# Kernel optimization log

Hardware: AMD Instinct MI355X
Metric: run time of the kernel (lower is better)

## Reference

```python
import jax, jax.numpy as jnp
import numpy as np

K = 512
H = 8
B = 8
T = 1024
EPS = 1e-5


def _layernorm(x, g, b):
    mu = jnp.mean(x, axis=-1, keepdims=True)
    var = jnp.var(x, axis=-1, keepdims=True)
    return (x - mu) * jax.lax.rsqrt(var + EPS) * g + b


def _attention(x, enc, wq, wk, wv, wo):
    b, t, k = x.shape
    h = H
    scale = k ** (-0.25)
    q = (x @ wq).reshape(b, t, h, k) * scale        # [b,t,h,k]
    kk = (enc @ wk).reshape(b, t, h, k) * scale
    v = (enc @ wv).reshape(b, t, h, k)
    dot = jnp.einsum('bqhd,bkhd->bhqk', q, kk)      # [b,h,t,t]
    att = jax.nn.softmax(dot, axis=-1)
    out = jnp.einsum('bhqk,bkhd->bqhd', att, v).reshape(b, t, h * k)
    return out @ wo                                  # [b,t,k]


def setup_inputs() -> dict:
    key = jax.random.key(0)
    ks = jax.random.split(key, 12)
    s = 0.02
    return {
        'x': jax.random.normal(ks[0], (B, T, K), jnp.float32),
        'enc': jax.random.normal(ks[1], (B, T, K), jnp.float32),
        'sa_wq': jax.random.normal(ks[2], (K, K * H), jnp.float32) * s,
        'sa_wk': jax.random.normal(ks[3], (K, K * H), jnp.float32) * s,
        'sa_wv': jax.random.normal(ks[4], (K, K * H), jnp.float32) * s,
        'sa_wo': jax.random.normal(ks[5], (K * H, K), jnp.float32) * s,
        'ca_wq': jax.random.normal(ks[6], (K, K * H), jnp.float32) * s,
        'ca_wk': jax.random.normal(ks[7], (K, K * H), jnp.float32) * s,
        'ca_wv': jax.random.normal(ks[8], (K, K * H), jnp.float32) * s,
        'ca_wo': jax.random.normal(ks[9], (K * H, K), jnp.float32) * s,
        'ln1_g': jnp.ones((K,), jnp.float32), 'ln1_b': jnp.zeros((K,), jnp.float32),
        'ln2_g': jnp.ones((K,), jnp.float32), 'ln2_b': jnp.zeros((K,), jnp.float32),
        'ln3_g': jnp.ones((K,), jnp.float32), 'ln3_b': jnp.zeros((K,), jnp.float32),
        'ff_w1': jax.random.normal(ks[10], (K, 4 * K), jnp.float32) * s,
        'ff_b1': jnp.zeros((4 * K,), jnp.float32),
        'ff_w2': jax.random.normal(ks[11], (4 * K, K), jnp.float32) * s,
        'ff_b2': jnp.zeros((K,), jnp.float32),
    }


def reference(x, enc, sa_wq, sa_wk, sa_wv, sa_wo, ca_wq, ca_wk, ca_wv, ca_wo,
              ln1_g, ln1_b, ln2_g, ln2_b, ln3_g, ln3_b,
              ff_w1, ff_b1, ff_w2, ff_b2):
    # masked self-attention (mask_future_steps=False -> plain self-attn)
    sa = _attention(x, x, sa_wq, sa_wk, sa_wv, sa_wo)
    x = _layernorm(sa + x, ln1_g, ln1_b)
    # encoder-decoder attention
    ca = _attention(x, enc, ca_wq, ca_wk, ca_wv, ca_wo)
    x = _layernorm(ca + x, ln2_g, ln2_b)
    # dropout p=0.0 -> identity
    ff = jax.nn.relu(x @ ff_w1 + ff_b1) @ ff_w2 + ff_b2
    x = _layernorm(ff + x, ln3_g, ln3_b)
    return x
```

## Files before the change

kernel.cpp:

```cpp
#include <hip/hip_runtime.h>
#include <stdint.h>

typedef short short8 __attribute__((ext_vector_type(8)));
typedef float f32x4 __attribute__((ext_vector_type(4)));

#define DEVI static __device__ __forceinline__

DEVI float b2f(unsigned short u) {
  union { float f; uint32_t i; } v; v.i = ((uint32_t)u) << 16; return v.f;
}
DEVI unsigned short f2b(float f) {
  union { float f; uint32_t i; } v; v.f = f;
  uint32_t r = v.i + 0x7FFFu + ((v.i >> 16) & 1u);
  return (unsigned short)(r >> 16);
}

DEVI void async_cp16(const unsigned short* g, unsigned short* l) {
  __builtin_amdgcn_global_load_lds(
      (const __attribute__((address_space(1))) void*)g,
      (__attribute__((address_space(3))) void*)l, 16, 0, 0);
}

DEVI void swz(int& bx, int& by, int& bz) {
  const int gx = gridDim.x, gy = gridDim.y, gz = gridDim.z;
  int l = blockIdx.x + gx * (blockIdx.y + gy * blockIdx.z);
  bz = l % gz; l /= gz;
  by = l % gy;
  bx = l / gy;
}


__global__ __launch_bounds__(256) void cvt_f32_bf16(
    const float4* __restrict__ src, unsigned short* __restrict__ dst) {
  const int i = blockIdx.x * 256 + threadIdx.x;
  float4 f = src[i];
  uint2 o;
  o.x = (uint32_t)f2b(f.x) | ((uint32_t)f2b(f.y) << 16);
  o.y = (uint32_t)f2b(f.z) | ((uint32_t)f2b(f.w) << 16);
  ((uint2*)dst)[i] = o;
}

__global__ __launch_bounds__(256) void wtrans(
    const float* __restrict__ src, unsigned short* __restrict__ dst, int R, int C) {
  __shared__ float tile[32][33];
  const int tx = threadIdx.x & 31, ty = threadIdx.x >> 5;
  const int c0 = blockIdx.x * 32, r0 = blockIdx.y * 32;
#pragma unroll
  for (int i = 0; i < 32; i += 8)
    tile[ty + i][tx] = src[(long)(r0 + ty + i) * C + c0 + tx];
  __syncthreads();
#pragma unroll
  for (int i = 0; i < 32; i += 8)
    dst[(long)(c0 + ty + i) * R + r0 + tx] = f2b(tile[tx][ty + i]);
}

__global__ __launch_bounds__(256) void softmax_rows(
    unsigned short* __restrict__ S, int NZ) {
  const int tid = threadIdx.x;
  const int bx = blockIdx.x;
  const long z = bx % NZ, r = bx / NZ;
  unsigned short* p = S + (z * 1024 + r) * 1024;
  float v[4];
  float m = -3.0e38f;
#pragma unroll
  for (int i = 0; i < 4; i++) { v[i] = b2f(p[tid + 256 * i]); m = fmaxf(m, v[i]); }
#pragma unroll
  for (int o = 1; o < 64; o <<= 1) m = fmaxf(m, __shfl_xor(m, o));
  __shared__ float rm[4], rsum[4];
  const int lane = tid & 63, wave = tid >> 6;
  if (lane == 0) rm[wave] = m;
  __syncthreads();
  m = fmaxf(fmaxf(rm[0], rm[1]), fmaxf(rm[2], rm[3]));
  float s = 0.f;
#pragma unroll
  for (int i = 0; i < 4; i++) { v[i] = __expf(v[i] - m); s += v[i]; }
#pragma unroll
  for (int o = 1; o < 64; o <<= 1) s += __shfl_xor(s, o);
  if (lane == 0) rsum[wave] = s;
  __syncthreads();
  s = rsum[0] + rsum[1] + rsum[2] + rsum[3];
  const float inv = 1.f / s;
#pragma unroll
  for (int i = 0; i < 4; i++) p[tid + 256 * i] = f2b(v[i] * inv);
}

__global__ __launch_bounds__(256) void layernorm_rows(
    const float* X, const float* __restrict__ g,
    const float* __restrict__ b, float* Y,
    unsigned short* __restrict__ Yb) {
  const int tid = threadIdx.x;
  const long row = blockIdx.x;
  const float* x = X + row * 512;
  float v0 = x[tid], v1 = x[tid + 256];
  float s1 = v0 + v1;
  float s2 = v0 * v0 + v1 * v1;
#pragma unroll
  for (int o = 1; o < 64; o <<= 1) {
    s1 += __shfl_xor(s1, o);
    s2 += __shfl_xor(s2, o);
  }
  __shared__ float r1[4], r2[4];
  const int lane = tid & 63, wave = tid >> 6;
  if (lane == 0) { r1[wave] = s1; r2[wave] = s2; }
  __syncthreads();
  s1 = r1[0] + r1[1] + r1[2] + r1[3];
  s2 = r2[0] + r2[1] + r2[2] + r2[3];
  const float mu = s1 * (1.f / 512.f);
  const float var = s2 * (1.f / 512.f) - mu * mu;
  const float rs = rsqrtf(var + 1e-5f);
  float y0 = (v0 - mu) * rs * g[tid] + b[tid];
  float y1 = (v1 - mu) * rs * g[tid + 256] + b[tid + 256];
  if (Y) { Y[row * 512 + tid] = y0; Y[row * 512 + tid + 256] = y1; }
  if (Yb) { Yb[row * 512 + tid] = f2b(y0); Yb[row * 512 + tid + 256] = f2b(y1); }
}

template <int EPI>
__global__ __launch_bounds__(256, 2) void gemm_bt(
    const unsigned short* __restrict__ A, int lda, long asb, long ash,
    const unsigned short* __restrict__ B, int ldb, long bsb, long bsh,
    void* Cv, int ldc, long csb, long csh,
    int K, float scale,
    const float* __restrict__ bias, const float* res) {
  __shared__ __align__(16) unsigned short As[128 * 32];
  __shared__ __align__(16) unsigned short Bs[128 * 32];
  int bx, by, bz;
  swz(bx, by, bz);
  const int tid = threadIdx.x;
  const int lane = tid & 63;
  const int wave = tid >> 6;
  const int zb = bz >> 3, zh = bz & 7;
  const int m0 = by * 128;
  const int n0 = bx * 128;

  const unsigned short* Ab = A + zb * asb + zh * ash + (long)m0 * lda;
  const unsigned short* Bb = B + zb * bsb + zh * bsh + (long)n0 * ldb;

  const int r0 = tid >> 2;
  const int p0 = (tid & 3) << 3;

  f32x4 acc[4][4];
#pragma unroll
  for (int i = 0; i < 4; i++)
#pragma unroll
    for (int j = 0; j < 4; j++) acc[i][j] = (f32x4){0.f, 0.f, 0.f, 0.f};

  const int wm = (wave >> 1) << 6;
  const int wn = (wave & 1) << 6;
  const int fm = lane & 15;
  const int k8 = (lane >> 4) << 3;

  for (int kt = 0; kt < K; kt += 32) {
    __syncthreads();
    async_cp16(Ab + (long)r0 * lda + kt + p0, &As[tid * 8]);
    async_cp16(Ab + (long)(r0 + 64) * lda + kt + p0, &As[2048 + tid * 8]);
    async_cp16(Bb + (long)r0 * ldb + kt + p0, &Bs[tid * 8]);
    async_cp16(Bb + (long)(r0 + 64) * ldb + kt + p0, &Bs[2048 + tid * 8]);
    __syncthreads();

    short8 af[4], bfr[4];
#pragma unroll
    for (int i = 0; i < 4; i++)
      af[i] = *(const short8*)&As[(wm + i * 16 + fm) * 32 + k8];
#pragma unroll
    for (int j = 0; j < 4; j++)
      bfr[j] = *(const short8*)&Bs[(wn + j * 16 + fm) * 32 + k8];
#pragma unroll
    for (int i = 0; i < 4; i++)
#pragma unroll
      for (int j = 0; j < 4; j++)
        acc[i][j] = __builtin_amdgcn_mfma_f32_16x16x32_bf16(af[i], bfr[j], acc[i][j], 0, 0, 0);
  }

  const long coff = zb * csb + zh * csh;
  const int er = (lane >> 4) << 2;
  const int ec = lane & 15;
#pragma unroll
  for (int i = 0; i < 4; i++) {
#pragma unroll
    for (int j = 0; j < 4; j++) {
      const int gc = n0 + wn + j * 16 + ec;
#pragma unroll
      for (int r = 0; r < 4; r++) {
        const int gr = m0 + wm + i * 16 + er + r;
        const float v = acc[i][j][r];
        const long idx = coff + (long)gr * ldc + gc;
        if constexpr (EPI == 0) {
          ((unsigned short*)Cv)[idx] = f2b(v * scale);
        } else if constexpr (EPI == 1) {
          float o = v;
          if (bias) o += bias[gc];
          if (res) o += res[(long)gr * ldc + gc];
          ((float*)Cv)[idx] = o;
        } else {
          ((unsigned short*)Cv)[idx] = f2b(fmaxf(v + bias[gc], 0.f));
        }
      }
    }
  }
}

extern "C" void kernel_launch(void* const* d_in, const int* in_sizes, int n_in,
                              void* d_out, int out_size, void* d_ws, size_t ws_size,
                              hipStream_t stream) {
  const float* x     = (const float*)d_in[0];
  const float* enc   = (const float*)d_in[1];
  const float* ln1_g = (const float*)d_in[10];
  const float* ln1_b = (const float*)d_in[11];
  const float* ln2_g = (const float*)d_in[12];
  const float* ln2_b = (const float*)d_in[13];
  const float* ln3_g = (const float*)d_in[14];
  const float* ln3_b = (const float*)d_in[15];
  const float* ff_b1 = (const float*)d_in[17];
  const float* ff_b2 = (const float*)d_in[19];

  uint8_t* ws = (uint8_t*)d_ws;
  auto US = [&](size_t o) { return (unsigned short*)(ws + o); };
  auto F  = [&](size_t o) { return (float*)(ws + o); };

  const size_t MB = 1ull << 20;
  const size_t SZ_WBIG = 4 * MB, SZ_WFF = 2 * MB;

  const size_t O_XB = 0, O_ENCB = 8 * MB, O_WT = 16 * MB;
  const size_t O_RES = 52 * MB;
  const size_t O_XNB = 68 * MB;
  auto WT = [&](int i) { return US(O_WT + (size_t)i * SZ_WBIG); };

  int HP = 1;
  for (int c = 8; c >= 1; c >>= 1)
    if (ws_size >= (76 + 40 * (size_t)c) * MB) { HP = c; break; }
  const int NG = 8 / HP;
  const int NZ = HP * 8;
  const int LD = HP * 512;
  const size_t O_QG  = 76 * MB;
  const size_t O_KG  = O_QG + (size_t)HP * 8 * MB;
  const size_t O_VTG = O_KG + (size_t)HP * 8 * MB;
  const size_t O_SG  = O_VTG + (size_t)HP * 8 * MB;
  const size_t O_H   = 76 * MB;

  const float qsc = 0.21022410381342863f;
  dim3 B256(256);

  cvt_f32_bf16<<<4096, B256, 0, stream>>>((const float4*)x, US(O_XB));
  cvt_f32_bf16<<<4096, B256, 0, stream>>>((const float4*)enc, US(O_ENCB));

  struct WSpec { const float* s; size_t off; int R, C; };
  const WSpec wspec[10] = {
      {(const float*)d_in[2], O_WT + 0 * SZ_WBIG, 512, 4096},
      {(const float*)d_in[3], O_WT + 1 * SZ_WBIG, 512, 4096},
      {(const float*)d_in[4], O_WT + 2 * SZ_WBIG, 512, 4096},
      {(const float*)d_in[5], O_WT + 3 * SZ_WBIG, 4096, 512},
      {(const float*)d_in[6], O_WT + 4 * SZ_WBIG, 512, 4096},
      {(const float*)d_in[7], O_WT + 5 * SZ_WBIG, 512, 4096},
      {(const float*)d_in[8], O_WT + 6 * SZ_WBIG, 512, 4096},
      {(const float*)d_in[9], O_WT + 7 * SZ_WBIG, 4096, 512},
      {(const float*)d_in[16], O_WT + 8 * SZ_WBIG, 512, 2048},
      {(const float*)d_in[18], O_WT + 8 * SZ_WBIG + SZ_WFF, 2048, 512},
  };
  for (int i = 0; i < 10; i++)
    wtrans<<<dim3(wspec[i].C / 32, wspec[i].R / 32), B256, 0, stream>>>(
        wspec[i].s, US(wspec[i].off), wspec[i].R, wspec[i].C);

  auto attention = [&](const unsigned short* qsrc, const unsigned short* kvsrc,
                       int wb, const float* resid) {
    for (int g = 0; g < NG; g++) {
      const size_t woff = (size_t)g * LD * 512;
      gemm_bt<0><<<dim3(HP * 4, 64, 1), B256, 0, stream>>>(
          qsrc, 512, 0, 0, WT(wb + 0) + woff, 512, 0, 0,
          US(O_QG), LD, 0, 0, 512, qsc, nullptr, nullptr);
      gemm_bt<0><<<dim3(HP * 4, 64, 1), B256, 0, stream>>>(
          kvsrc, 512, 0, 0, WT(wb + 1) + woff, 512, 0, 0,
          US(O_KG), LD, 0, 0, 512, qsc, nullptr, nullptr);
      gemm_bt<0><<<dim3(64, HP * 4, 1), B256, 0, stream>>>(
          WT(wb + 2) + woff, 512, 0, 0, kvsrc, 512, 0, 0,
          US(O_VTG), 8192, 0, 0, 512, 1.f, nullptr, nullptr);
      gemm_bt<0><<<dim3(8, 8, NZ), B256, 0, stream>>>(
          US(O_QG), LD, 512L, (long)1024 * LD,
          US(O_KG), LD, 512L, (long)1024 * LD,
          US(O_SG), 1024, 8388608L, 1048576L, 512, 1.f, nullptr, nullptr);
      softmax_rows<<<NZ * 1024, B256, 0, stream>>>(US(O_SG), NZ);
      gemm_bt<0><<<dim3(4, 8, NZ), B256, 0, stream>>>(
          US(O_SG), 1024, 8388608L, 1048576L,
          US(O_VTG), 8192, 4194304L, 1024L,
          US(O_QG), LD, 512L, (long)1024 * LD, 1024, 1.f, nullptr, nullptr);
      gemm_bt<1><<<dim3(4, 64, 1), B256, 0, stream>>>(
          US(O_QG), LD, 0, 0, WT(wb + 3) + (size_t)g * LD, 4096, 0, 0,
          F(O_RES), 512, 0, 0, LD, 1.f, nullptr, g == 0 ? resid : F(O_RES));
    }
  };

  attention(US(O_XB), US(O_XB), 0, x);
  layernorm_rows<<<8192, B256, 0, stream>>>(F(O_RES), ln1_g, ln1_b, F(O_RES), US(O_XNB));
  attention(US(O_XNB), US(O_ENCB), 4, F(O_RES));
  layernorm_rows<<<8192, B256, 0, stream>>>(F(O_RES), ln2_g, ln2_b, F(O_RES), US(O_XNB));
  gemm_bt<2><<<dim3(16, 64, 1), B256, 0, stream>>>(
      US(O_XNB), 512, 0, 0, WT(8), 512, 0, 0,
      US(O_H), 2048, 0, 0, 512, 1.f, ff_b1, nullptr);
  gemm_bt<1><<<dim3(4, 64, 1), B256, 0, stream>>>(
      US(O_H), 2048, 0, 0, US(O_WT + 8 * SZ_WBIG + SZ_WFF), 2048, 0, 0,
      F(O_RES), 512, 0, 0, 2048, 1.f, ff_b2, F(O_RES));
  layernorm_rows<<<8192, B256, 0, stream>>>(F(O_RES), ln3_g, ln3_b, (float*)d_out, nullptr);
}
```

Baseline: 1.337 ms.

## Double-buffer GEMM LDS tiles and use 64-row tiles for narrow outputs

The bf16 MFMA GEMM now keeps two LDS buffers. It issues the async global-to-LDS copy for the next K-slice before computing on the current one, so each K step needs one barrier instead of two and loads overlap MFMA work. The kernel is templated on the M tile size. The output-projection and FFN2 GEMMs, whose N is only 512, now use 64-row tiles, which doubles their block count and fills the GPU better. The costs are twice the LDS per block and a risk that the compiler inserts conservative vmcnt waits that undo the overlap.

After: 1.244 ms. -6.9%, faster.

```diff
diff --git a/kernel.cpp b/kernel.cpp
--- a/kernel.cpp
+++ b/kernel.cpp
@@ -114,22 +114,23 @@
   if (Yb) { Yb[row * 512 + tid] = f2b(y0); Yb[row * 512 + tid + 256] = f2b(y1); }
 }
 
-template <int EPI>
+template <int EPI, int BM>
 __global__ __launch_bounds__(256, 2) void gemm_bt(
     const unsigned short* __restrict__ A, int lda, long asb, long ash,
     const unsigned short* __restrict__ B, int ldb, long bsb, long bsh,
     void* Cv, int ldc, long csb, long csh,
     int K, float scale,
     const float* __restrict__ bias, const float* res) {
-  __shared__ __align__(16) unsigned short As[128 * 32];
-  __shared__ __align__(16) unsigned short Bs[128 * 32];
+  constexpr int MI = BM / 32;
+  __shared__ __align__(16) unsigned short As[2][BM * 32];
+  __shared__ __align__(16) unsigned short Bs[2][128 * 32];
   int bx, by, bz;
   swz(bx, by, bz);
   const int tid = threadIdx.x;
   const int lane = tid & 63;
   const int wave = tid >> 6;
   const int zb = bz >> 3, zh = bz & 7;
-  const int m0 = by * 128;
+  const int m0 = by * BM;
   const int n0 = bx * 128;
 
   const unsigned short* Ab = A + zb * asb + zh * ash + (long)m0 * lda;
@@ -138,44 +139,54 @@
   const int r0 = tid >> 2;
   const int p0 = (tid & 3) << 3;
 
-  f32x4 acc[4][4];
-#pragma unroll
-  for (int i = 0; i < 4; i++)
+  f32x4 acc[MI][4];
+#pragma unroll
+  for (int i = 0; i < MI; i++)
 #pragma unroll
     for (int j = 0; j < 4; j++) acc[i][j] = (f32x4){0.f, 0.f, 0.f, 0.f};
 
-  const int wm = (wave >> 1) << 6;
+  const int wm = (wave >> 1) * (BM / 2);
   const int wn = (wave & 1) << 6;
   const int fm = lane & 15;
   const int k8 = (lane >> 4) << 3;
 
-  for (int kt = 0; kt < K; kt += 32) {
-    __syncthreads();
-    async_cp16(Ab + (long)r0 * lda + kt + p0, &As[tid * 8]);
-    async_cp16(Ab + (long)(r0 + 64) * lda + kt + p0, &As[2048 + tid * 8]);
-    async_cp16(Bb + (long)r0 * ldb + kt + p0, &Bs[tid * 8]);
-    async_cp16(Bb + (long)(r0 + 64) * ldb + kt + p0, &Bs[2048 + tid * 8]);
-    __syncthreads();
-
-    short8 af[4], bfr[4];
-#pragma unroll
-    for (int i = 0; i < 4; i++)
-      af[i] = *(const short8*)&As[(wm + i * 16 + fm) * 32 + k8];
+  auto stage = [&](int buf, int kt) {
+    async_cp16(Ab + (long)r0 * lda + kt + p0, &As[buf][tid * 8]);
+    if constexpr (BM == 128)
+      async_cp16(Ab + (long)(r0 + 64) * lda + kt + p0, &As[buf][2048 + tid * 8]);
+    async_cp16(Bb + (long)r0 * ldb + kt + p0, &Bs[buf][tid * 8]);
+    async_cp16(Bb + (long)(r0 + 64) * ldb + kt + p0, &Bs[buf][2048 + tid * 8]);
+  };
+
+  const int nt = K >> 5;
+  stage(0, 0);
+  __syncthreads();
+  int cur = 0;
+  for (int t = 0; t < nt; ++t) {
+    if (t + 1 < nt) stage(cur ^ 1, (t + 1) << 5);
+
+    short8 af[MI], bfr[4];
+#pragma unroll
+    for (int i = 0; i < MI; i++)
+      af[i] = *(const short8*)&As[cur][(wm + i * 16 + fm) * 32 + k8];
 #pragma unroll
     for (int j = 0; j < 4; j++)
-      bfr[j] = *(const short8*)&Bs[(wn + j * 16 + fm) * 32 + k8];
-#pragma unroll
-    for (int i = 0; i < 4; i++)
+      bfr[j] = *(const short8*)&Bs[cur][(wn + j * 16 + fm) * 32 + k8];
+#pragma unroll
+    for (int i = 0; i < MI; i++)
 #pragma unroll
       for (int j = 0; j < 4; j++)
         acc[i][j] = __builtin_amdgcn_mfma_f32_16x16x32_bf16(af[i], bfr[j], acc[i][j], 0, 0, 0);
+
+    __syncthreads();
+    cur ^= 1;
   }
 
   const long coff = zb * csb + zh * csh;
   const int er = (lane >> 4) << 2;
   const int ec = lane & 15;
 #pragma unroll
-  for (int i = 0; i < 4; i++) {
+  for (int i = 0; i < MI; i++) {
 #pragma unroll
     for (int j = 0; j < 4; j++) {
       const int gc = n0 + wn + j * 16 + ec;
@@ -264,25 +275,25 @@
                        int wb, const float* resid) {
     for (int g = 0; g < NG; g++) {
       const size_t woff = (size_t)g * LD * 512;
-      gemm_bt<0><<<dim3(HP * 4, 64, 1), B256, 0, stream>>>(
+      gemm_bt<0, 128><<<dim3(HP * 4, 64, 1), B256, 0, stream>>>(
           qsrc, 512, 0, 0, WT(wb + 0) + woff, 512, 0, 0,
           US(O_QG), LD, 0, 0, 512, qsc, nullptr, nullptr);
-      gemm_bt<0><<<dim3(HP * 4, 64, 1), B256, 0, stream>>>(
+      gemm_bt<0, 128><<<dim3(HP * 4, 64, 1), B256, 0, stream>>>(
           kvsrc, 512, 0, 0, WT(wb + 1) + woff, 512, 0, 0,
           US(O_KG), LD, 0, 0, 512, qsc, nullptr, nullptr);
-      gemm_bt<0><<<dim3(64, HP * 4, 1), B256, 0, stream>>>(
+      gemm_bt<0, 128><<<dim3(64, HP * 4, 1), B256, 0, stream>>>(
           WT(wb + 2) + woff, 512, 0, 0, kvsrc, 512, 0, 0,
           US(O_VTG), 8192, 0, 0, 512, 1.f, nullptr, nullptr);
-      gemm_bt<0><<<dim3(8, 8, NZ), B256, 0, stream>>>(
+      gemm_bt<0, 128><<<dim3(8, 8, NZ), B256, 0, stream>>>(
           US(O_QG), LD, 512L, (long)1024 * LD,
           US(O_KG), LD, 512L, (long)1024 * LD,
           US(O_SG), 1024, 8388608L, 1048576L, 512, 1.f, nullptr, nullptr);
       softmax_rows<<<NZ * 1024, B256, 0, stream>>>(US(O_SG), NZ);
-      gemm_bt<0><<<dim3(4, 8, NZ), B256, 0, stream>>>(
+      gemm_bt<0, 128><<<dim3(4, 8, NZ), B256, 0, stream>>>(
           US(O_SG), 1024, 8388608L, 1048576L,
           US(O_VTG), 8192, 4194304L, 1024L,
           US(O_QG), LD, 512L, (long)1024 * LD, 1024, 1.f, nullptr, nullptr);
-      gemm_bt<1><<<dim3(4, 64, 1), B256, 0, stream>>>(
+      gemm_bt<1, 64><<<dim3(4, 128, 1), B256, 0, stream>>>(
           US(O_QG), LD, 0, 0, WT(wb + 3) + (size_t)g * LD, 4096, 0, 0,
           F(O_RES), 512, 0, 0, LD, 1.f, nullptr, g == 0 ? resid : F(O_RES));
     }
@@ -292,10 +303,10 @@
   layernorm_rows<<<8192, B256, 0, stream>>>(F(O_RES), ln1_g, ln1_b, F(O_RES), US(O_XNB));
   attention(US(O_XNB), US(O_ENCB), 4, F(O_RES));
   layernorm_rows<<<8192, B256, 0, stream>>>(F(O_RES), ln2_g, ln2_b, F(O_RES), US(O_XNB));
-  gemm_bt<2><<<dim3(16, 64, 1), B256, 0, stream>>>(
+  gemm_bt<2, 128><<<dim3(16, 64, 1), B256, 0, stream>>>(
       US(O_XNB), 512, 0, 0, WT(8), 512, 0, 0,
       US(O_H), 2048, 0, 0, 512, 1.f, ff_b1, nullptr);
-  gemm_bt<1><<<dim3(4, 64, 1), B256, 0, stream>>>(
+  gemm_bt<1, 64><<<dim3(4, 128, 1), B256, 0, stream>>>(
       US(O_H), 2048, 0, 0, US(O_WT + 8 * SZ_WBIG + SZ_WFF), 2048, 0, 0,
       F(O_RES), 512, 0, 0, 2048, 1.f, ff_b2, F(O_RES));
   layernorm_rows<<<8192, B256, 0, stream>>>(F(O_RES), ln3_g, ln3_b, (float*)d_out, nullptr);
```
